# Kernel tuning notes

Measured on AMD Instinct MI355X. Metric: run time of the kernel, lower is better.

The kernel has to match this reference:

```python
import jax, jax.numpy as jnp
import numpy as np

EMBED_DIM = 1024
NUM_HEADS = 16
HEAD_DIM = EMBED_DIM // NUM_HEADS
B, N = 4, 2048
EPS = 1e-5


def rotate_half(x):
    x2d = x.reshape(x.shape[:-1] + (-1, 2))
    x1, x2 = x2d[..., 0], x2d[..., 1]
    return jnp.stack([-x2, x1], axis=-1).reshape(x.shape)


def apply_rotary_emb(freqs, t):
    return t * freqs[0] + rotate_half(t) * freqs[1]


def setup_inputs() -> dict:
    key = jax.random.key(0)
    ks = jax.random.split(key, 12)
    d = EMBED_DIM
    inp = {
        "x": jax.random.normal(ks[0], (B, N, d), jnp.float32),
        "encoding": jax.random.normal(ks[1], (2, N, HEAD_DIM), jnp.float32),
        "Wqkv_w": jax.random.normal(ks[2], (d, 3 * d), jnp.float32) * (1.0 / np.sqrt(d)),
        "Wqkv_b": jnp.zeros((3 * d,), jnp.float32),
        "out_w": jax.random.normal(ks[3], (d, d), jnp.float32) * (1.0 / np.sqrt(d)),
        "out_b": jnp.zeros((d,), jnp.float32),
        "ffn0_w": jax.random.normal(ks[4], (2 * d, 2 * d), jnp.float32) * (1.0 / np.sqrt(2 * d)),
        "ffn0_b": jnp.zeros((2 * d,), jnp.float32),
        "ln_scale": jnp.ones((2 * d,), jnp.float32),
        "ln_bias": jnp.zeros((2 * d,), jnp.float32),
        "ffn3_w": jax.random.normal(ks[5], (2 * d, d), jnp.float32) * (1.0 / np.sqrt(2 * d)),
        "ffn3_b": jnp.zeros((d,), jnp.float32),
    }
    return inp


def reference(x, encoding, Wqkv_w, Wqkv_b, out_w, out_b, ffn0_w, ffn0_b, ln_scale, ln_bias, ffn3_w, ffn3_b):
    b, n, d = x.shape
    # fused QKV projection
    qkv = jnp.einsum('bnd,de->bne', x, Wqkv_w) + Wqkv_b
    qkv = qkv.reshape(b, n, NUM_HEADS, HEAD_DIM, 3).transpose(0, 2, 1, 3, 4)  # (b,h,n,hd,3)
    q, k, v = qkv[..., 0], qkv[..., 1], qkv[..., 2]
    # RoPE (encoding broadcasts over batch/heads)
    q = apply_rotary_emb(encoding, q)
    k = apply_rotary_emb(encoding, k)
    # attention (no mask)
    scale = 1.0 / jnp.sqrt(jnp.asarray(HEAD_DIM, x.dtype))
    logits = jnp.einsum('bhqd,bhkd->bhqk', q, k) * scale
    attn = jax.nn.softmax(logits, axis=-1)
    context = jnp.einsum('bhqk,bhkd->bhqd', attn, v)
    message = context.transpose(0, 2, 1, 3).reshape(b, n, d)
    message = jnp.einsum('bnd,de->bne', message, out_w) + out_b
    # FFN: concat -> Dense -> LayerNorm -> GELU(exact) -> Dense
    h = jnp.concatenate([x, message], axis=-1)
    h = jnp.einsum('bnd,de->bne', h, ffn0_w) + ffn0_b
    mu = jnp.mean(h, axis=-1, keepdims=True)
    var = jnp.mean(jnp.square(h - mu), axis=-1, keepdims=True)
    h = (h - mu) * jax.lax.rsqrt(var + EPS) * ln_scale + ln_bias
    h = jax.nn.gelu(h, approximate=False)
    res = jnp.einsum('bnd,de->bne', h, ffn3_w) + ffn3_b
    return x + res
```

## Files before the change

### kernel.cpp

```cpp
#include <hip/hip_runtime.h>
#include <hip/hip_bf16.h>
#include <math.h>

typedef __bf16 bf16x8 __attribute__((ext_vector_type(8)));
typedef float f32x4 __attribute__((ext_vector_type(4)));

#define MFMA16(a, b, c) __builtin_amdgcn_mfma_f32_16x16x32_bf16((a), (b), (c), 0, 0, 0)

__device__ __forceinline__ void gload16(const void* g, void* l) {
  __builtin_amdgcn_global_load_lds((const __attribute__((address_space(1))) void*)g,
                                   (__attribute__((address_space(3))) void*)l, 16, 0, 0);
}

#define BARRIER asm volatile("s_barrier" ::: "memory")

__global__ __launch_bounds__(256) void transpose_bf16(const float* __restrict__ in,
                                                      int ldin,
                                                      __bf16* __restrict__ out,
                                                      int ldo) {
  __shared__ float tile[32][33];
  int n0 = blockIdx.x * 32, k0 = blockIdx.y * 32;
  int tx = threadIdx.x & 31, ty = threadIdx.x >> 5;
#pragma unroll
  for (int r = 0; r < 32; r += 8)
    tile[ty + r][tx] = in[(size_t)(k0 + ty + r) * ldin + n0 + tx];
  __syncthreads();
#pragma unroll
  for (int r = 0; r < 32; r += 8)
    out[(size_t)(n0 + ty + r) * ldo + k0 + tx] = (__bf16)tile[tx][ty + r];
}

__global__ __launch_bounds__(256) void transpose_qkv_perm(const float* __restrict__ in,
                                                          __bf16* __restrict__ out) {
  __shared__ float tile[32][33];
  int n0 = blockIdx.x * 32, k0 = blockIdx.y * 32;
  int tx = threadIdx.x & 31, ty = threadIdx.x >> 5;
#pragma unroll
  for (int r = 0; r < 32; r += 8)
    tile[ty + r][tx] = in[(size_t)(k0 + ty + r) * 3072 + n0 + tx];
  __syncthreads();
#pragma unroll
  for (int r = 0; r < 32; r += 8) {
    int n = n0 + ty + r;
    int h = n / 192, rem = n % 192, hd = rem / 3, which = rem % 3;
    int np = which * 1024 + h * 64 + hd;
    out[(size_t)np * 1024 + k0 + tx] = (__bf16)tile[tx][ty + r];
  }
}

__global__ __launch_bounds__(256) void bias_perm(const float* __restrict__ b,
                                                 float* __restrict__ bp) {
  int n = blockIdx.x * 256 + threadIdx.x;
  if (n < 3072) {
    int h = n / 192, rem = n % 192, hd = rem / 3, which = rem % 3;
    bp[which * 1024 + h * 64 + hd] = b[n];
  }
}

__global__ __launch_bounds__(256) void convert_plain(const float* __restrict__ in,
                                                     __bf16* __restrict__ out) {
  int id = blockIdx.x * 256 + threadIdx.x;
  const float* src = in + (size_t)id * 8;
  __bf16 tmp[8];
#pragma unroll
  for (int e = 0; e < 8; ++e) tmp[e] = (__bf16)src[e];
  *(uint4*)(out + (size_t)id * 8) = *(uint4*)tmp;
}

__global__ __launch_bounds__(256) void convert_x(const float* __restrict__ x,
                                                 __bf16* __restrict__ h) {
  int id = blockIdx.x * 256 + threadIdx.x;
  int row = id >> 7, cc = id & 127;
  const float* src = x + (size_t)row * 1024 + cc * 8;
  __bf16 tmp[8];
#pragma unroll
  for (int e = 0; e < 8; ++e) tmp[e] = (__bf16)src[e];
  *(uint4*)(h + (size_t)row * 2048 + cc * 8) = *(uint4*)tmp;
}

__global__ __launch_bounds__(256) void fuse_bias_part(const float* __restrict__ bout,
                                                      const float* __restrict__ w0,
                                                      float* __restrict__ part) {
  int n = blockIdx.x * 256 + threadIdx.x;
  int e0 = blockIdx.y * 64;
  float s = 0.f;
#pragma unroll 4
  for (int e = 0; e < 64; ++e)
    s += bout[e0 + e] * w0[(size_t)(1024 + e0 + e) * 2048 + n];
  part[(size_t)blockIdx.y * 2048 + n] = s;
}

__global__ __launch_bounds__(256) void fuse_bias_red(const float* __restrict__ part,
                                                     const float* __restrict__ b0,
                                                     float* __restrict__ bf) {
  int n = blockIdx.x * 256 + threadIdx.x;
  float s = b0[n];
#pragma unroll
  for (int y = 0; y < 16; ++y) s += part[(size_t)y * 2048 + n];
  bf[n] = s;
}

template <typename OutT, bool HAS_RES, bool HAS_BIAS>
__global__ __launch_bounds__(256) void gemm_kernel(
    const __bf16* __restrict__ A, int lda,
    const __bf16* __restrict__ Bt,
    const float* __restrict__ bias,
    OutT* __restrict__ C, int ldc,
    const float* __restrict__ res,
    int M, int Nn, int K) {
  __shared__ __attribute__((aligned(16))) __bf16 As[128 * 64];
  __shared__ __attribute__((aligned(16))) __bf16 Bs[128 * 64];

  const int t = threadIdx.x;
  const int row0A = blockIdx.x * 128;
  const int row0B = blockIdx.y * 128;
  const int wave = t >> 6, lane = t & 63;
  const int wm = wave >> 1, wn = wave & 1;
  const int g = lane >> 4, lr = lane & 15;

  f32x4 acc[4][4] = {};

  for (int k0 = 0; k0 < K; k0 += 64) {
#pragma unroll
    for (int p = 0; p < 4; ++p) {
      int cbase = (wave * 4 + p) * 64;
      int ci = cbase + lane;
      int r = ci >> 3, cp = ci & 7, cl = cp ^ (r & 7);
      gload16(A + (size_t)(row0A + r) * lda + k0 + cl * 8, &As[cbase * 8]);
      gload16(Bt + (size_t)(row0B + r) * K + k0 + cl * 8, &Bs[cbase * 8]);
    }
    __syncthreads();
#pragma unroll
    for (int kk = 0; kk < 2; ++kk) {
      bf16x8 af[4], bfr[4];
#pragma unroll
      for (int mt = 0; mt < 4; ++mt) {
        int r = wm * 64 + mt * 16 + lr, c = kk * 4 + g;
        af[mt] = *(const bf16x8*)((char*)As + r * 128 + ((c ^ (r & 7)) * 16));
      }
#pragma unroll
      for (int nt = 0; nt < 4; ++nt) {
        int r = wn * 64 + nt * 16 + lr, c = kk * 4 + g;
        bfr[nt] = *(const bf16x8*)((char*)Bs + r * 128 + ((c ^ (r & 7)) * 16));
      }
#pragma unroll
      for (int mt = 0; mt < 4; ++mt)
#pragma unroll
        for (int nt = 0; nt < 4; ++nt)
          acc[mt][nt] = MFMA16(af[mt], bfr[nt], acc[mt][nt]);
    }
    __syncthreads();
  }

  float bias_v[4];
#pragma unroll
  for (int nt = 0; nt < 4; ++nt)
    bias_v[nt] = HAS_BIAS ? bias[row0B + wn * 64 + nt * 16 + lr] : 0.f;
#pragma unroll
  for (int mt = 0; mt < 4; ++mt) {
    int grow_base = row0A + wm * 64 + mt * 16 + g * 4;
#pragma unroll
    for (int nt = 0; nt < 4; ++nt) {
      int gcol = row0B + wn * 64 + nt * 16 + lr;
#pragma unroll
      for (int j = 0; j < 4; ++j) {
        int grow = grow_base + j;
        float v = acc[mt][nt][j] + bias_v[nt];
        if (HAS_RES) v += res[(size_t)grow * ldc + gcol];
        C[(size_t)grow * ldc + gcol] = (OutT)v;
      }
    }
  }
}

template <typename OutT>
__global__ __launch_bounds__(512, 2) void gemm256p(
    const __bf16* __restrict__ A, int lda,
    const __bf16* __restrict__ Bt, int ldb,
    const float* __restrict__ bias,
    OutT* __restrict__ C, int ldc, int K) {
  __shared__ __attribute__((aligned(16))) __bf16 As[2][256 * 64];
  __shared__ __attribute__((aligned(16))) __bf16 Bs[2][256 * 64];

  const int t = threadIdx.x;
  const int wave = t >> 6, lane = t & 63;
  const int wm = wave >> 2, wn = wave & 3;
  const int g = lane >> 4, lr = lane & 15;
  const int row0A = blockIdx.x * 256, row0B = blockIdx.y * 256;
  const int L = K >> 6;

  f32x4 acc[8][4] = {};

#define STG_A(tile, i)                                                        \
  {                                                                           \
    int cb = ((i) * 8 + wave) * 64;                                           \
    int ci = cb + lane;                                                       \
    int r = ci >> 3, cl = (ci & 7) ^ (r & 7);                                 \
    gload16(A + (size_t)(row0A + r) * lda + (size_t)(tile) * 64 + cl * 8,     \
            &As[(tile) & 1][cb * 8]);                                         \
  }
#define STG_B(tile, i)                                                        \
  {                                                                           \
    int cb = ((i) * 8 + wave) * 64;                                           \
    int ci = cb + lane;                                                       \
    int r = ci >> 3, cl = (ci & 7) ^ (r & 7);                                 \
    gload16(Bt + (size_t)(row0B + r) * ldb + (size_t)(tile) * 64 + cl * 8,    \
            &Bs[(tile) & 1][cb * 8]);                                         \
  }
#define AFRAG(d, mi, ks)                                                      \
  (*(const bf16x8*)((const char*)As[d] + (wm * 128 + (mi) * 16 + lr) * 128 +  \
                    ((((ks) * 4 + g) ^ (lr & 7)) * 16)))
#define BFRAG(d, ni, ks)                                                      \
  (*(const bf16x8*)((const char*)Bs[d] + (wn * 64 + (ni) * 16 + lr) * 128 +   \
                    ((((ks) * 4 + g) ^ (lr & 7)) * 16)))

#pragma unroll
  for (int i = 0; i < 4; ++i) STG_A(0, i);
#pragma unroll
  for (int i = 0; i < 4; ++i) STG_B(0, i);
  STG_A(1, 0);
  STG_A(1, 1);
  asm volatile("s_waitcnt vmcnt(2)" ::: "memory");
  BARRIER;

  for (int tt = 0; tt < L; ++tt) {
    const int d = tt & 1;
    const bool s1 = (tt + 1) < L, s2 = (tt + 2) < L;
    bf16x8 aL[4][2], aH[4][2], bL[2][2], bH[2][2];

#pragma unroll
    for (int mi = 0; mi < 4; ++mi) {
      aL[mi][0] = AFRAG(d, mi, 0);
      aL[mi][1] = AFRAG(d, mi, 1);
    }
#pragma unroll
    for (int ni = 0; ni < 2; ++ni) {
      bL[ni][0] = BFRAG(d, ni, 0);
      bL[ni][1] = BFRAG(d, ni, 1);
    }
    if (s1) { STG_A(tt + 1, 2); STG_A(tt + 1, 3); }
    BARRIER;
    __builtin_amdgcn_s_setprio(1);
#pragma unroll
    for (int mi = 0; mi < 4; ++mi)
#pragma unroll
      for (int ni = 0; ni < 2; ++ni) {
        acc[mi][ni] = MFMA16(aL[mi][0], bL[ni][0], acc[mi][ni]);
        acc[mi][ni] = MFMA16(aL[mi][1], bL[ni][1], acc[mi][ni]);
      }
    __builtin_amdgcn_s_setprio(0);
    BARRIER;

#pragma unroll
    for (int ni = 0; ni < 2; ++ni) {
      bH[ni][0] = BFRAG(d, ni + 2, 0);
      bH[ni][1] = BFRAG(d, ni + 2, 1);
    }
    if (s1) { STG_B(tt + 1, 0); STG_B(tt + 1, 1); }
    BARRIER;
    __builtin_amdgcn_s_setprio(1);
#pragma unroll
    for (int mi = 0; mi < 4; ++mi)
#pragma unroll
      for (int ni = 0; ni < 2; ++ni) {
        acc[mi][ni + 2] = MFMA16(aL[mi][0], bH[ni][0], acc[mi][ni + 2]);
        acc[mi][ni + 2] = MFMA16(aL[mi][1], bH[ni][1], acc[mi][ni + 2]);
      }
    __builtin_amdgcn_s_setprio(0);
    BARRIER;

#pragma unroll
    for (int mi = 0; mi < 4; ++mi) {
      aH[mi][0] = AFRAG(d, mi + 4, 0);
      aH[mi][1] = AFRAG(d, mi + 4, 1);
    }
    if (s1) { STG_B(tt + 1, 2); STG_B(tt + 1, 3); }
    BARRIER;
    __builtin_amdgcn_s_setprio(1);
#pragma unroll
    for (int mi = 0; mi < 4; ++mi)
#pragma unroll
      for (int ni = 0; ni < 2; ++ni) {
        acc[mi + 4][ni + 2] = MFMA16(aH[mi][0], bH[ni][0], acc[mi + 4][ni + 2]);
        acc[mi + 4][ni + 2] = MFMA16(aH[mi][1], bH[ni][1], acc[mi + 4][ni + 2]);
      }
    __builtin_amdgcn_s_setprio(0);
    BARRIER;

    if (s2) { STG_A(tt + 2, 0); STG_A(tt + 2, 1); }
    __builtin_amdgcn_s_setprio(1);
#pragma unroll
    for (int mi = 0; mi < 4; ++mi)
#pragma unroll
      for (int ni = 0; ni < 2; ++ni) {
        acc[mi + 4][ni] = MFMA16(aH[mi][0], bL[ni][0], acc[mi + 4][ni]);
        acc[mi + 4][ni] = MFMA16(aH[mi][1], bL[ni][1], acc[mi + 4][ni]);
      }
    __builtin_amdgcn_s_setprio(0);
    if (s2)
      asm volatile("s_waitcnt vmcnt(2)" ::: "memory");
    else
      asm volatile("s_waitcnt vmcnt(0)" ::: "memory");
    BARRIER;
  }
#undef STG_A
#undef STG_B
#undef AFRAG
#undef BFRAG

  float bias_v[4];
#pragma unroll
  for (int ni = 0; ni < 4; ++ni) bias_v[ni] = bias[row0B + wn * 64 + ni * 16 + lr];
#pragma unroll
  for (int mi = 0; mi < 8; ++mi) {
    int grow_base = row0A + wm * 128 + mi * 16 + g * 4;
#pragma unroll
    for (int ni = 0; ni < 4; ++ni) {
      int gcol = row0B + wn * 64 + ni * 16 + lr;
#pragma unroll
      for (int j = 0; j < 4; ++j)
        C[(size_t)(grow_base + j) * ldc + gcol] = (OutT)(acc[mi][ni][j] + bias_v[ni]);
    }
  }
}

__global__ __launch_bounds__(256) void rope_scatter(
    const __bf16* __restrict__ qkv, const float* __restrict__ enc,
    __bf16* __restrict__ q, __bf16* __restrict__ kk, __bf16* __restrict__ vt) {
  int bh = blockIdx.y;
  int b = bh >> 4, h = bh & 15;
  int n0 = blockIdx.x * 64;
  int t = threadIdx.x;
  const float QSC = 0.125f * 1.44269504088896f;
#pragma unroll
  for (int i = 0; i < 2; ++i) {
    int id = t + i * 256;
    int nl = id >> 3, cc = id & 7;
    int n = n0 + nl;
    size_t row = (size_t)(b * 2048 + n) * 3072;
    bf16x8 qv = *(const bf16x8*)(qkv + row + h * 64 + cc * 8);
    bf16x8 kv = *(const bf16x8*)(qkv + row + 1024 + h * 64 + cc * 8);
    const float* e0 = enc + (size_t)n * 64 + cc * 8;
    const float* e1 = e0 + 131072;
    __bf16 qo[8], ko[8];
#pragma unroll
    for (int e = 0; e < 8; e += 2) {
      float q0 = (float)qv[e], q1 = (float)qv[e + 1];
      float k0 = (float)kv[e], k1 = (float)kv[e + 1];
      float f00 = e0[e], f01 = e0[e + 1], f10 = e1[e], f11 = e1[e + 1];
      qo[e] = (__bf16)((q0 * f00 - q1 * f10) * QSC);
      qo[e + 1] = (__bf16)((q1 * f01 + q0 * f11) * QSC);
      ko[e] = (__bf16)(k0 * f00 - k1 * f10);
      ko[e + 1] = (__bf16)(k1 * f01 + k0 * f11);
    }
    size_t qb = ((size_t)bh * 2048 + n) * 64 + cc * 8;
    *(uint4*)(q + qb) = *(uint4*)qo;
    *(uint4*)(kk + qb) = *(uint4*)ko;
  }
#pragma unroll
  for (int i = 0; i < 2; ++i) {
    int id = t + i * 256;
    int hd = id >> 3, c = id & 7;
    __bf16 tmp[8];
#pragma unroll
    for (int e = 0; e < 8; ++e) {
      int kv = (c >> 2) * 32 + (e >> 2) * 16 + (c & 3) * 4 + (e & 3);
      int n = n0 + kv;
      tmp[e] = qkv[(size_t)(b * 2048 + n) * 3072 + 2048 + h * 64 + hd];
    }
    *(uint4*)(vt + ((size_t)bh * 64 + hd) * 2048 + n0 + c * 8) = *(uint4*)tmp;
  }
}

__global__ __launch_bounds__(256) void attn_kernel(
    const __bf16* __restrict__ q, const __bf16* __restrict__ k,
    const __bf16* __restrict__ vt, __bf16* __restrict__ ctx) {
  __shared__ __attribute__((aligned(16))) __bf16 Ks[2][64 * 64];
  __shared__ __attribute__((aligned(16))) __bf16 Vs[2][64 * 64];

  int nwg = gridDim.x * gridDim.y;
  int bid0 = blockIdx.y * gridDim.x + blockIdx.x;
  int bid = (bid0 & 7) * (nwg >> 3) + (bid0 >> 3);
  const int bh = bid / gridDim.x, qblk = bid % gridDim.x;
  const int b = bh >> 4, h = bh & 15;
  const int q0 = qblk * 64;
  const int t = threadIdx.x, wave = t >> 6, lane = t & 63;
  const int g = lane >> 4, lr = lane & 15;
  const int qrow = q0 + wave * 16;

  const __bf16* kbase = k + (size_t)bh * 2048 * 64;
  const __bf16* vbase = vt + (size_t)bh * 64 * 2048;

  bf16x8 qf[2];
#pragma unroll
  for (int kc = 0; kc < 2; ++kc)
    qf[kc] = *(const bf16x8*)(q + ((size_t)bh * 2048 + qrow + lr) * 64 + kc * 32 + g * 8);

  bf16x8 ones;
#pragma unroll
  for (int e = 0; e < 8; ++e) ones[e] = (__bf16)1.0f;

  f32x4 o[4] = {};
  f32x4 lacc = {};

#define STAGE_ATTN(buf, kv0)                                                    \
  {                                                                             \
    _Pragma("unroll") for (int p = 0; p < 2; ++p) {                             \
      int cbase = wave * 128 + p * 64;                                          \
      int ci = cbase + lane;                                                    \
      int r = ci >> 3, cp = ci & 7, cl = cp ^ (r & 7);                          \
      gload16(kbase + (size_t)((kv0) + r) * 64 + cl * 8, &Ks[buf][cbase * 8]);  \
      gload16(vbase + (size_t)r * 2048 + (kv0) + cl * 8, &Vs[buf][cbase * 8]);  \
    }                                                                           \
  }

  STAGE_ATTN(0, 0);
  __syncthreads();
  int buf = 0;

  for (int kv0 = 0; kv0 < 2048; kv0 += 64) {
    if (kv0 + 64 < 2048) STAGE_ATTN(buf ^ 1, kv0 + 64);

    f32x4 s[4];
    __builtin_amdgcn_s_setprio(1);
#pragma unroll
    for (int nt = 0; nt < 4; ++nt) {
      int r = nt * 16 + lr;
      bf16x8 kf0 = *(const bf16x8*)((char*)Ks[buf] + r * 128 + ((g ^ (r & 7)) * 16));
      bf16x8 kf1 = *(const bf16x8*)((char*)Ks[buf] + r * 128 + (((4 + g) ^ (r & 7)) * 16));
      f32x4 a = {};
      a = MFMA16(kf0, qf[0], a);
      a = MFMA16(kf1, qf[1], a);
      s[nt] = a;
    }
    __builtin_amdgcn_s_setprio(0);

#pragma unroll
    for (int t2 = 0; t2 < 2; ++t2) {
      bf16x8 pf;
#pragma unroll
      for (int e = 0; e < 8; ++e)
        pf[e] = (__bf16)__builtin_amdgcn_exp2f(s[2 * t2 + (e >> 2)][e & 3]);
      lacc = MFMA16(ones, pf, lacc);
      __builtin_amdgcn_s_setprio(1);
#pragma unroll
      for (int nt = 0; nt < 4; ++nt) {
        int r = nt * 16 + lr;
        bf16x8 vf = *(const bf16x8*)((char*)Vs[buf] + r * 128 + (((t2 * 4 + g) ^ (r & 7)) * 16));
        o[nt] = MFMA16(vf, pf, o[nt]);
      }
      __builtin_amdgcn_s_setprio(0);
    }
    __syncthreads();
    buf ^= 1;
  }

  float inv = 1.f / lacc[0];

  size_t obase = ((size_t)(b * 2048 + qrow + lr)) * 2048 + 1024 + h * 64;
#pragma unroll
  for (int nt = 0; nt < 4; ++nt) {
    __bf16 w4[4];
#pragma unroll
    for (int j = 0; j < 4; ++j) w4[j] = (__bf16)(o[nt][j] * inv);
    *(uint2*)(ctx + obase + nt * 16 + g * 4) = *(uint2*)w4;
  }
#undef STAGE_ATTN
}

__global__ __launch_bounds__(256) void ln_gelu(const __bf16* __restrict__ hin,
                                               const float* __restrict__ lns,
                                               const float* __restrict__ lnb,
                                               __bf16* __restrict__ hout) {
  int row = blockIdx.x;
  const __bf16* rp = hin + (size_t)row * 2048;
  int t = threadIdx.x;
  __bf16 tmp[8];
  *(uint4*)tmp = *(const uint4*)(rp + t * 8);
  float vals[8], s = 0.f, s2 = 0.f;
#pragma unroll
  for (int e = 0; e < 8; ++e) {
    float x = (float)tmp[e];
    vals[e] = x;
    s += x;
    s2 += x * x;
  }
#pragma unroll
  for (int m = 1; m < 64; m <<= 1) {
    s += __shfl_xor(s, m, 64);
    s2 += __shfl_xor(s2, m, 64);
  }
  __shared__ float red[8];
  int wave = t >> 6, lane = t & 63;
  if (lane == 0) { red[wave] = s; red[4 + wave] = s2; }
  __syncthreads();
  s = red[0] + red[1] + red[2] + red[3];
  s2 = red[4] + red[5] + red[6] + red[7];
  float mu = s * (1.f / 2048.f);
  float var = s2 * (1.f / 2048.f) - mu * mu;
  float rstd = rsqrtf(var + 1e-5f);
  __bf16 outv[8];
#pragma unroll
  for (int e = 0; e < 8; ++e) {
    int c = t * 8 + e;
    float xh = (vals[e] - mu) * rstd * lns[c] + lnb[c];
    float gg = 0.5f * xh * (1.f + erff(xh * 0.70710678118f));
    outv[e] = (__bf16)gg;
  }
  *(uint4*)(hout + (size_t)row * 2048 + t * 8) = *(uint4*)outv;
}

extern "C" void kernel_launch(void* const* d_in, const int* in_sizes, int n_in,
                              void* d_out, int out_size, void* d_ws, size_t ws_size,
                              hipStream_t stream) {
  const float* x = (const float*)d_in[0];
  const float* enc = (const float*)d_in[1];
  const float* wqkv = (const float*)d_in[2];
  const float* bqkv = (const float*)d_in[3];
  const float* wout = (const float*)d_in[4];
  const float* bout = (const float*)d_in[5];
  const float* wffn0 = (const float*)d_in[6];
  const float* bffn0 = (const float*)d_in[7];
  const float* lns = (const float*)d_in[8];
  const float* lnb = (const float*)d_in[9];
  const float* wffn3 = (const float*)d_in[10];
  const float* bffn3 = (const float*)d_in[11];
  float* out = (float*)d_out;
  char* ws = (char*)d_ws;

  __bf16* wT_qkv = (__bf16*)(ws + 0);
  __bf16* wT_ffn0 = (__bf16*)(ws + 6291456);
  __bf16* wT_ffn3 = (__bf16*)(ws + 14680064);
  __bf16* wout_bf = (__bf16*)(ws + 18874368);
  __bf16* w0bT = (__bf16*)(ws + 20971520);
  float* bias_part = (float*)(ws + 20971520);
  float* bqkv_p = (float*)(ws + 25165824);
  float* bffn0_f = (float*)(ws + 25178112);
  __bf16* h_in = (__bf16*)(ws + 25186304);
  __bf16* qkv = (__bf16*)(ws + 58740736);
  __bf16* ffn0o = qkv;
  __bf16* qb = (__bf16*)(ws + 109072384);
  __bf16* h2 = qb;
  __bf16* kb = (__bf16*)(ws + 125849600);
  __bf16* vtb = (__bf16*)(ws + 142626816);

  dim3 blk(256);
  transpose_qkv_perm<<<dim3(96, 32), blk, 0, stream>>>(wqkv, wT_qkv);
  bias_perm<<<12, blk, 0, stream>>>(bqkv, bqkv_p);
  transpose_bf16<<<dim3(64, 32), blk, 0, stream>>>(wffn0, 2048, wT_ffn0, 2048);
  transpose_bf16<<<dim3(64, 32), blk, 0, stream>>>(wffn0 + (size_t)1024 * 2048, 2048,
                                                   w0bT, 1024);
  transpose_bf16<<<dim3(32, 64), blk, 0, stream>>>(wffn3, 1024, wT_ffn3, 2048);
  convert_plain<<<512, blk, 0, stream>>>(wout, wout_bf);
  gemm_kernel<__bf16, false, false><<<dim3(16, 8), blk, 0, stream>>>(
      w0bT, 1024, wout_bf, nullptr, wT_ffn0 + 1024, 2048, nullptr, 2048, 1024, 1024);
  fuse_bias_part<<<dim3(8, 16), blk, 0, stream>>>(bout, wffn0, bias_part);
  fuse_bias_red<<<8, blk, 0, stream>>>(bias_part, bffn0, bffn0_f);
  convert_x<<<4096, blk, 0, stream>>>(x, h_in);

  gemm256p<__bf16><<<dim3(32, 12), dim3(512), 0, stream>>>(
      h_in, 2048, wT_qkv, 1024, bqkv_p, qkv, 3072, 1024);

  rope_scatter<<<dim3(32, 64), blk, 0, stream>>>(qkv, enc, qb, kb, vtb);
  attn_kernel<<<dim3(32, 64), blk, 0, stream>>>(qb, kb, vtb, h_in);

  gemm256p<__bf16><<<dim3(32, 8), dim3(512), 0, stream>>>(
      h_in, 2048, wT_ffn0, 2048, bffn0_f, ffn0o, 2048, 2048);

  ln_gelu<<<8192, blk, 0, stream>>>(ffn0o, lns, lnb, h2);

  gemm_kernel<float, true, true><<<dim3(64, 8), blk, 0, stream>>>(
      h2, 2048, wT_ffn3, bffn3, out, 1024, x, 8192, 1024, 2048);
}
```

Measured before the change: 405.1 us.

## Double attention query tile per workgroup to reuse K/V tiles across two row blocks

Each wave now processes two 16-row query blocks, so a workgroup covers 128 queries and the grid is halved. Every K and V fragment read from LDS feeds two MFMAs, which halves global K/V staging traffic and LDS reads per query. The cost is more accumulator registers (two sets of o, s, lacc), which may lower occupancy, and half as many workgroups to spread over the CUs.

```diff
diff --git a/kernel.cpp b/kernel.cpp
--- a/kernel.cpp
+++ b/kernel.cpp
@@ -381,27 +381,30 @@
   int nwg = gridDim.x * gridDim.y;
   int bid0 = blockIdx.y * gridDim.x + blockIdx.x;
   int bid = (bid0 & 7) * (nwg >> 3) + (bid0 >> 3);
-  const int bh = bid / gridDim.x, qblk = bid % gridDim.x;
+  const int bh = bid >> 4, qblk = bid & 15;
   const int b = bh >> 4, h = bh & 15;
-  const int q0 = qblk * 64;
+  const int q0 = qblk * 128;
   const int t = threadIdx.x, wave = t >> 6, lane = t & 63;
   const int g = lane >> 4, lr = lane & 15;
-  const int qrow = q0 + wave * 16;
+  const int qrow0 = q0 + wave * 32;
 
   const __bf16* kbase = k + (size_t)bh * 2048 * 64;
   const __bf16* vbase = vt + (size_t)bh * 64 * 2048;
 
-  bf16x8 qf[2];
-#pragma unroll
-  for (int kc = 0; kc < 2; ++kc)
-    qf[kc] = *(const bf16x8*)(q + ((size_t)bh * 2048 + qrow + lr) * 64 + kc * 32 + g * 8);
+  bf16x8 qf[2][2];
+#pragma unroll
+  for (int u = 0; u < 2; ++u)
+#pragma unroll
+    for (int kc = 0; kc < 2; ++kc)
+      qf[u][kc] = *(const bf16x8*)(q + ((size_t)bh * 2048 + qrow0 + u * 16 + lr) * 64 +
+                                   kc * 32 + g * 8);
 
   bf16x8 ones;
 #pragma unroll
   for (int e = 0; e < 8; ++e) ones[e] = (__bf16)1.0f;
 
-  f32x4 o[4] = {};
-  f32x4 lacc = {};
+  f32x4 o[2][4] = {};
+  f32x4 lacc[2] = {};
 
 #define STAGE_ATTN(buf, kv0)                                                    \
   {                                                                             \
@@ -421,33 +424,40 @@
   for (int kv0 = 0; kv0 < 2048; kv0 += 64) {
     if (kv0 + 64 < 2048) STAGE_ATTN(buf ^ 1, kv0 + 64);
 
-    f32x4 s[4];
+    f32x4 s[2][4];
     __builtin_amdgcn_s_setprio(1);
 #pragma unroll
     for (int nt = 0; nt < 4; ++nt) {
       int r = nt * 16 + lr;
       bf16x8 kf0 = *(const bf16x8*)((char*)Ks[buf] + r * 128 + ((g ^ (r & 7)) * 16));
       bf16x8 kf1 = *(const bf16x8*)((char*)Ks[buf] + r * 128 + (((4 + g) ^ (r & 7)) * 16));
-      f32x4 a = {};
-      a = MFMA16(kf0, qf[0], a);
-      a = MFMA16(kf1, qf[1], a);
-      s[nt] = a;
+#pragma unroll
+      for (int u = 0; u < 2; ++u) {
+        f32x4 a = {};
+        a = MFMA16(kf0, qf[u][0], a);
+        a = MFMA16(kf1, qf[u][1], a);
+        s[u][nt] = a;
+      }
     }
     __builtin_amdgcn_s_setprio(0);
 
 #pragma unroll
     for (int t2 = 0; t2 < 2; ++t2) {
-      bf16x8 pf;
-#pragma unroll
-      for (int e = 0; e < 8; ++e)
-        pf[e] = (__bf16)__builtin_amdgcn_exp2f(s[2 * t2 + (e >> 2)][e & 3]);
-      lacc = MFMA16(ones, pf, lacc);
+      bf16x8 pf[2];
+#pragma unroll
+      for (int u = 0; u < 2; ++u) {
+#pragma unroll
+        for (int e = 0; e < 8; ++e)
+          pf[u][e] = (__bf16)__builtin_amdgcn_exp2f(s[u][2 * t2 + (e >> 2)][e & 3]);
+        lacc[u] = MFMA16(ones, pf[u], lacc[u]);
+      }
       __builtin_amdgcn_s_setprio(1);
 #pragma unroll
       for (int nt = 0; nt < 4; ++nt) {
         int r = nt * 16 + lr;
         bf16x8 vf = *(const bf16x8*)((char*)Vs[buf] + r * 128 + (((t2 * 4 + g) ^ (r & 7)) * 16));
-        o[nt] = MFMA16(vf, pf, o[nt]);
+#pragma unroll
+        for (int u = 0; u < 2; ++u) o[u][nt] = MFMA16(vf, pf[u], o[u][nt]);
       }
       __builtin_amdgcn_s_setprio(0);
     }
@@ -455,15 +465,17 @@
     buf ^= 1;
   }
 
-  float inv = 1.f / lacc[0];
-
-  size_t obase = ((size_t)(b * 2048 + qrow + lr)) * 2048 + 1024 + h * 64;
-#pragma unroll
-  for (int nt = 0; nt < 4; ++nt) {
-    __bf16 w4[4];
-#pragma unroll
-    for (int j = 0; j < 4; ++j) w4[j] = (__bf16)(o[nt][j] * inv);
-    *(uint2*)(ctx + obase + nt * 16 + g * 4) = *(uint2*)w4;
+#pragma unroll
+  for (int u = 0; u < 2; ++u) {
+    float inv = 1.f / lacc[u][0];
+    size_t obase = ((size_t)(b * 2048 + qrow0 + u * 16 + lr)) * 2048 + 1024 + h * 64;
+#pragma unroll
+    for (int nt = 0; nt < 4; ++nt) {
+      __bf16 w4[4];
+#pragma unroll
+      for (int j = 0; j < 4; ++j) w4[j] = (__bf16)(o[u][nt][j] * inv);
+      *(uint2*)(ctx + obase + nt * 16 + g * 4) = *(uint2*)w4;
+    }
   }
 #undef STAGE_ATTN
 }
@@ -562,7 +574,7 @@
       h_in, 2048, wT_qkv, 1024, bqkv_p, qkv, 3072, 1024);
 
   rope_scatter<<<dim3(32, 64), blk, 0, stream>>>(qkv, enc, qb, kb, vtb);
-  attn_kernel<<<dim3(32, 64), blk, 0, stream>>>(qb, kb, vtb, h_in);
+  attn_kernel<<<dim3(16, 64), blk, 0, stream>>>(qb, kb, vtb, h_in);
 
   gemm256p<__bf16><<<dim3(32, 8), dim3(512), 0, stream>>>(
       h_in, 2048, wT_ffn0, 2048, bffn0_f, ffn0o, 2048, 2048);
```

Measured after the change: 393.7 us. 2.8% less time.
